# Optimization experiments

Hardware: AMD Instinct MI355X
Metric: run time of the kernel (lower is better)

Reference implementation:

```python
import jax, jax.numpy as jnp
import numpy as np

N_EMBD = 1024
N_HEAD = 16
HEAD_DIM = N_EMBD // N_HEAD


def setup_inputs() -> dict:
    key = jax.random.key(0)
    ks = jax.random.split(key, 9)
    B, S = 4, 2048
    s = 1.0 / np.sqrt(N_EMBD)
    return {
        "x": jax.random.normal(ks[0], (B, S, N_EMBD), dtype=jnp.float32),
        "attention_mask": jnp.ones((B, S), dtype=jnp.int32),
        "Wq": jax.random.normal(ks[1], (N_EMBD, N_EMBD), jnp.float32) * s,
        "bq": jnp.zeros((N_EMBD,), jnp.float32),
        "Wk": jax.random.normal(ks[2], (N_EMBD, N_EMBD), jnp.float32) * s,
        "bk": jnp.zeros((N_EMBD,), jnp.float32),
        "Wv": jax.random.normal(ks[3], (N_EMBD, N_EMBD), jnp.float32) * s,
        "bv": jnp.zeros((N_EMBD,), jnp.float32),
        "Wo": jax.random.normal(ks[4], (N_EMBD, N_EMBD), jnp.float32) * s,
        "bo": jnp.zeros((N_EMBD,), jnp.float32),
    }


def _split_heads(t):  # [B,S,E] -> [B,H,S,D]
    B, S, _ = t.shape
    return t.reshape(B, S, N_HEAD, HEAD_DIM).transpose(0, 2, 1, 3)


def reference(x, attention_mask, Wq, bq, Wk, bk, Wv, bv, Wo, bo):
    B, S, E = x.shape
    q = _split_heads(x @ Wq.T + bq)
    k = _split_heads(x @ Wk.T + bk)
    v = _split_heads(x @ Wv.T + bv)
    # scores: [B,H,S,S]
    scores = jnp.einsum('bhqd,bhkd->bhqk', q, k) / np.sqrt(HEAD_DIM).astype(np.float32)
    # additive mask: 0 where mask==1, -inf where mask==0, broadcast over heads/query
    mask = jnp.where(attention_mask[:, None, None, :] == 0, -jnp.inf, 0.0).astype(scores.dtype)
    scores = scores + mask
    probs = jax.nn.softmax(scores, axis=-1)  # dropout p=0 -> identity
    ctx = jnp.einsum('bhqk,bhkd->bhqd', probs, v)
    out = ctx.transpose(0, 2, 1, 3).reshape(B, S, E)
    return out @ Wo.T + bo
```

## Files before the change

kernel.cpp:

```cpp
#include <hip/hip_runtime.h>

typedef __bf16 bf16;
typedef __attribute__((ext_vector_type(2))) bf16 bf16x2;
typedef __attribute__((ext_vector_type(4))) bf16 bf16x4;
typedef __attribute__((ext_vector_type(8))) bf16 bf16x8;
typedef __attribute__((ext_vector_type(4))) float f32x4;
typedef __attribute__((ext_vector_type(16))) float f32x16;
typedef __attribute__((ext_vector_type(4))) int i32x4;
typedef __attribute__((ext_vector_type(2))) int i32x2;

#define MFMA_BF16(a, b, c) __builtin_amdgcn_mfma_f32_16x16x32_bf16((a), (b), (c), 0, 0, 0)
#define MFMA32(a, b, c)    __builtin_amdgcn_mfma_f32_32x32x16_bf16((a), (b), (c), 0, 0, 0)

constexpr int S_LEN = 2048;
constexpr int EMB   = 1024;
constexpr int NHEAD = 16;
constexpr int HDIM  = 64;
constexpr int BATCH = 4;
constexpr int NTOK  = BATCH * S_LEN;

__device__ __forceinline__ void gload_lds16(const bf16* g, bf16* l) {
    __builtin_amdgcn_global_load_lds(
        (const __attribute__((address_space(1))) void*)g,
        (__attribute__((address_space(3))) void*)l, 16, 0, 0);
}

__device__ __forceinline__ int pkbf(float a, float b) {
    bf16x2 t; t[0] = (bf16)a; t[1] = (bf16)b;
    return __builtin_bit_cast(int, t);
}

#if __has_builtin(__builtin_amdgcn_permlane32_swap)
__device__ __forceinline__ i32x2 permswap(int a, int b) {
    return __builtin_amdgcn_permlane32_swap(a, b, false, false);
}
#else
__device__ __forceinline__ i32x2 permswap(int a, int b) {
    int as = __shfl_xor(a, 32);
    int bs = __shfl_xor(b, 32);
    int hx_ = (threadIdx.x >> 5) & 1;
    i32x2 r;
    r[0] = hx_ ? bs : a;
    r[1] = hx_ ? b : as;
    return r;
}
#endif

__global__ __launch_bounds__(256)
void cvt_f32_bf16(const float* __restrict__ src, bf16* __restrict__ dst, int n4) {
    int i = blockIdx.x * 256 + threadIdx.x;
    if (i < n4) {
        f32x4 v = ((const f32x4*)src)[i];
        bf16x4 o;
        o[0] = (bf16)v[0]; o[1] = (bf16)v[1]; o[2] = (bf16)v[2]; o[3] = (bf16)v[3];
        ((bf16x4*)dst)[i] = o;
    }
}

__global__ __launch_bounds__(256)
void cvt_w4(const float* __restrict__ s0, const float* __restrict__ s1,
            const float* __restrict__ s2, const float* __restrict__ s3,
            bf16* __restrict__ dst) {
    const int a = blockIdx.y;
    const float* s = a == 0 ? s0 : (a == 1 ? s1 : (a == 2 ? s2 : s3));
    int i = blockIdx.x * 256 + threadIdx.x;
    f32x4 v = ((const f32x4*)s)[i];
    bf16x4 o;
    o[0] = (bf16)v[0]; o[1] = (bf16)v[1]; o[2] = (bf16)v[2]; o[3] = (bf16)v[3];
    ((bf16x4*)(dst + (size_t)a * EMB * EMB))[i] = o;
}

__global__ __launch_bounds__(512)
void gemm256(const bf16* __restrict__ A,
             const bf16* __restrict__ W0, const bf16* __restrict__ W1, const bf16* __restrict__ W2,
             const float* __restrict__ b0, const float* __restrict__ b1, const float* __restrict__ b2,
             void* __restrict__ d0, void* __restrict__ d1, void* __restrict__ d2,
             int fused, float q_scale)
{
    __shared__ bf16 lds[2][4][8192];

    int seg, mode, n0;
    if (fused) { seg = blockIdx.y >> 2; n0 = (blockIdx.y & 3) * 256; mode = (seg == 2) ? 1 : 0; }
    else       { seg = 0;              n0 = blockIdx.y * 256;        mode = 2; }
    const bf16*  W    = seg == 0 ? W0 : (seg == 1 ? W1 : W2);
    const float* bias = seg == 0 ? b0 : (seg == 1 ? b1 : b2);
    void*        C    = seg == 0 ? d0 : (seg == 1 ? d1 : d2);
    const float  osc  = (fused && seg == 0) ? q_scale : 1.0f;

    const int tid  = threadIdx.x;
    const int lane = tid & 63;
    const int w    = tid >> 6;
    const int wr   = w >> 2;
    const int wc   = w & 3;
    const int quad = lane >> 4;
    const int l16  = lane & 15;
    const int m0   = blockIdx.x * 256;

#define STAGE_A(BUF, H, T) {                                                        \
    _Pragma("unroll") for (int c_ = 0; c_ < 2; ++c_) {                              \
        int idx_ = c_ * 512 + tid;                                                  \
        int m_ = idx_ >> 2, s_ = idx_ & 3;                                          \
        gload_lds16(A + (size_t)(m0 + m_) * EMB + (T) * 64 + (H) * 32               \
                      + ((s_ ^ ((m_ >> 1) & 3)) << 3),                              \
                    &lds[BUF][H][idx_ * 8]);                                        \
    } }
#define STAGE_B(BUF, H, T) {                                                        \
    _Pragma("unroll") for (int c_ = 0; c_ < 2; ++c_) {                              \
        int idx_ = c_ * 512 + tid;                                                  \
        int n_ = idx_ >> 2, s_ = idx_ & 3;                                          \
        gload_lds16(W + (size_t)(n0 + n_) * EMB + (T) * 64 + (H) * 32               \
                      + ((s_ ^ ((n_ >> 1) & 3)) << 3),                              \
                    &lds[BUF][2 + (H)][idx_ * 8]);                                  \
    } }

#define READ_A(DST, BUF, H, G) {                                                    \
    _Pragma("unroll") for (int i_ = 0; i_ < 4; ++i_) {                              \
        int m_ = wr * 128 + (G) * 64 + i_ * 16 + l16;                               \
        DST[i_] = *(const bf16x8*)&lds[BUF][H][m_ * 32 + ((quad ^ ((m_ >> 1) & 3)) << 3)]; \
    } }
#define READ_B(DST, BUF, H) {                                                       \
    _Pragma("unroll") for (int j_ = 0; j_ < 4; ++j_) {                              \
        int n_ = wc * 64 + j_ * 16 + l16;                                           \
        DST[j_] = *(const bf16x8*)&lds[BUF][2 + (H)][n_ * 32 + ((quad ^ ((n_ >> 1) & 3)) << 3)]; \
    } }

#define MFMA_PH(AF, BF, G) {                                                        \
    __builtin_amdgcn_s_setprio(1);                                                  \
    _Pragma("unroll") for (int i_ = 0; i_ < 4; ++i_)                                \
        _Pragma("unroll") for (int j_ = 0; j_ < 4; ++j_)                            \
            acc[(G) * 4 + i_][j_] = MFMA_BF16(AF[i_], BF[j_], acc[(G) * 4 + i_][j_]); \
    __builtin_amdgcn_s_setprio(0);                                                  \
}

    f32x4 acc[8][4] = {};

    STAGE_A(0, 0, 0) STAGE_B(0, 0, 0) STAGE_A(0, 1, 0) STAGE_B(0, 1, 0)
    asm volatile("s_waitcnt vmcnt(4)" ::: "memory");
    __builtin_amdgcn_s_barrier();
    __builtin_amdgcn_sched_barrier(0);

    for (int t = 0; t < 16; ++t) {
        const int cur  = t & 1;
        const int nxt  = cur ^ 1;
        const bool more = (t + 1 < 16);
        bf16x8 afr[4], bfr[4];

        READ_B(bfr, cur, 0)
        READ_A(afr, cur, 0, 0)
        if (more) STAGE_A(nxt, 0, t + 1)
        MFMA_PH(afr, bfr, 0)

        READ_A(afr, cur, 0, 1)
        if (more) STAGE_B(nxt, 0, t + 1)
        MFMA_PH(afr, bfr, 1)
        if (more) asm volatile("s_waitcnt vmcnt(4)" ::: "memory");
        else      asm volatile("s_waitcnt vmcnt(0)" ::: "memory");
        __builtin_amdgcn_s_barrier();
        __builtin_amdgcn_sched_barrier(0);

        READ_B(bfr, cur, 1)
        READ_A(afr, cur, 1, 0)
        if (more) STAGE_A(nxt, 1, t + 1)
        MFMA_PH(afr, bfr, 0)

        READ_A(afr, cur, 1, 1)
        if (more) STAGE_B(nxt, 1, t + 1)
        MFMA_PH(afr, bfr, 1)
        if (more) {
            asm volatile("s_waitcnt vmcnt(4)" ::: "memory");
            __builtin_amdgcn_s_barrier();
            __builtin_amdgcn_sched_barrier(0);
        }
    }

#undef STAGE_A
#undef STAGE_B
#undef READ_A
#undef READ_B
#undef MFMA_PH

    #pragma unroll
    for (int ii = 0; ii < 8; ++ii) {
        #pragma unroll
        for (int j = 0; j < 4; ++j) {
            int col = n0 + wc * 64 + j * 16 + l16;
            float bv = bias[col];
            int row0 = m0 + wr * 128 + ii * 16 + quad * 4;
            if (mode == 1) {
                int bb = row0 >> 11, s0 = row0 & 2047;
                int hh = col >> 6,   d  = col & 63;
                bf16x4 pk;
                #pragma unroll
                for (int r = 0; r < 4; ++r) pk[r] = (bf16)(acc[ii][j][r] + bv);
                *(bf16x4*)((bf16*)C + (size_t)((bb * NHEAD + hh) * HDIM + d) * S_LEN + s0) = pk;
            } else if (mode == 0) {
                #pragma unroll
                for (int r = 0; r < 4; ++r)
                    ((bf16*)C)[(size_t)(row0 + r) * EMB + col] = (bf16)((acc[ii][j][r] + bv) * osc);
            } else {
                #pragma unroll
                for (int r = 0; r < 4; ++r)
                    ((float*)C)[(size_t)(row0 + r) * EMB + col] = acc[ii][j][r] + bv;
            }
        }
    }
}

__global__ __launch_bounds__(512)
void flash_attn(const bf16* __restrict__ qg, const bf16* __restrict__ kg,
                const bf16* __restrict__ vtg, const int* __restrict__ maskg,
                bf16* __restrict__ ctx)
{
    __shared__ bf16  klds[2][64 * 64];
    __shared__ bf16  vlds[2][64 * 64];
    __shared__ bf16  bias_lds[2048];
    __shared__ float stat_lds[8][32];

    const int fb  = blockIdx.x;
    const int xcd = fb & 7;
    const int rr  = fb >> 3;
    const int qi  = rr & 7;
    const int gg  = rr >> 3;
    const int g   = gg * 8 + xcd;
    const int h   = g & 15;
    const int b   = g >> 4;
    const int q0  = qi * 256;

    const int tid  = threadIdx.x;
    const int lane = tid & 63;
    const int w    = tid >> 6;
    const int l32  = lane & 31;
    const int hx   = lane >> 5;

    const int srow  = tid >> 3;
    const int sslot = (tid & 7) ^ (srow & 7);

    int ok;
    {
        int i = tid * 4;
        i32x4 mv = *(const i32x4*)(maskg + b * S_LEN + i);
        bf16x4 bb;
        ok = 1;
        #pragma unroll
        for (int r = 0; r < 4; ++r) {
            ok &= (mv[r] != 0);
            bb[r] = mv[r] ? (bf16)0.f : (bf16)(-3.0e38f);
        }
        *(bf16x4*)&bias_lds[i] = bb;
    }
    const int allvalid = __syncthreads_and(ok);

    bf16x8 qf[4];
    {
        const bf16* qrow = qg + (size_t)(b * S_LEN + q0 + w * 32 + l32) * EMB + h * HDIM + hx * 8;
        qf[0] = *(const bf16x8*)(qrow);
        qf[1] = *(const bf16x8*)(qrow + 16);
        qf[2] = *(const bf16x8*)(qrow + 32);
        qf[3] = *(const bf16x8*)(qrow + 48);
    }

    const bf16* kgb = kg  + (size_t)b * S_LEN * EMB + h * HDIM;
    const bf16* vgb = vtg + (size_t)((b * NHEAD + h) * HDIM) * S_LEN;

    float mrow = -1e30f, lpart = 0.f;
    f32x16 o0, o1;
    #pragma unroll
    for (int r = 0; r < 16; ++r) { o0[r] = 0.f; o1[r] = 0.f; }

#define STAGE(BUF, KT) {                                                            \
    gload_lds16(kgb + (size_t)((KT) * 64 + srow) * EMB + sslot * 8,                 \
                &klds[BUF][tid * 8]);                                               \
    gload_lds16(vgb + (size_t)srow * S_LEN + (KT) * 64 + sslot * 8,                 \
                &vlds[BUF][tid * 8]);                                               \
}

#define LDSK(CUR, ROW, SB) (*(const bf16x8*)((const char*)&klds[CUR][0] + ((ROW) << 7) + ((((SB) ^ ((ROW) & 7))) << 4)))
#define LDSV(CUR, ROW, SB) (*(const bf16x8*)((const char*)&vlds[CUR][0] + ((ROW) << 7) + ((((SB) ^ ((ROW) & 7))) << 4)))

#define SUBTILE(CUR, KT, KK) {                                                      \
    f32x16 s_;                                                                      \
    _Pragma("unroll") for (int r_ = 0; r_ < 16; ++r_) s_[r_] = 0.f;                 \
    const int krow_ = (KK) * 32 + l32;                                              \
    __builtin_amdgcn_s_setprio(1);                                                  \
    s_ = MFMA32(LDSK(CUR, krow_, 0 * 2 + hx), qf[0], s_);                           \
    s_ = MFMA32(LDSK(CUR, krow_, 1 * 2 + hx), qf[1], s_);                           \
    s_ = MFMA32(LDSK(CUR, krow_, 2 * 2 + hx), qf[2], s_);                           \
    s_ = MFMA32(LDSK(CUR, krow_, 3 * 2 + hx), qf[3], s_);                           \
    __builtin_amdgcn_s_setprio(0);                                                  \
    if (!allvalid) {                                                                \
        _Pragma("unroll") for (int s4_ = 0; s4_ < 4; ++s4_) {                       \
            bf16x4 b4_ = *(const bf16x4*)&bias_lds[(KT) * 64 + (KK) * 32 + s4_ * 8 + hx * 4]; \
            _Pragma("unroll") for (int t_ = 0; t_ < 4; ++t_)                        \
                s_[4 * s4_ + t_] += (float)b4_[t_];                                 \
        }                                                                           \
    }                                                                               \
    float rmax_ = s_[0];                                                            \
    _Pragma("unroll") for (int r_ = 1; r_ < 16; ++r_) rmax_ = fmaxf(rmax_, s_[r_]); \
    rmax_ = fmaxf(rmax_, __shfl_xor(rmax_, 32));                                    \
    if (!__all(rmax_ <= mrow + 8.f)) {                                              \
        float mnew_  = fmaxf(mrow, rmax_);                                          \
        float alpha_ = __builtin_amdgcn_exp2f(mrow - mnew_);                        \
        mrow = mnew_; lpart *= alpha_;                                              \
        if (hx == 0) stat_lds[w][l32] = alpha_;                                     \
        _Pragma("unroll") for (int s4_ = 0; s4_ < 4; ++s4_) {                       \
            f32x4 a4_ = *(const f32x4*)&stat_lds[w][s4_ * 8 + hx * 4];              \
            _Pragma("unroll") for (int t_ = 0; t_ < 4; ++t_) {                      \
                o0[4 * s4_ + t_] *= a4_[t_]; o1[4 * s4_ + t_] *= a4_[t_];           \
            }                                                                       \
        }                                                                           \
    }                                                                               \
    bf16x8 pa0, pa1;                                                                \
    {                                                                               \
        float p_[8];                                                                \
        _Pragma("unroll") for (int r_ = 0; r_ < 8; ++r_) {                          \
            p_[r_] = __builtin_amdgcn_exp2f(s_[r_] - mrow); lpart += p_[r_];        \
        }                                                                           \
        i32x2 r0_ = permswap(pkbf(p_[0], p_[1]), pkbf(p_[4], p_[5]));               \
        i32x2 r1_ = permswap(pkbf(p_[2], p_[3]), pkbf(p_[6], p_[7]));               \
        i32x4 fw_; fw_[0] = r0_[0]; fw_[1] = r1_[0]; fw_[2] = r0_[1]; fw_[3] = r1_[1]; \
        pa0 = __builtin_bit_cast(bf16x8, fw_);                                      \
    }                                                                               \
    {                                                                               \
        float p_[8];                                                                \
        _Pragma("unroll") for (int r_ = 0; r_ < 8; ++r_) {                          \
            p_[r_] = __builtin_amdgcn_exp2f(s_[8 + r_] - mrow); lpart += p_[r_];    \
        }                                                                           \
        i32x2 r0_ = permswap(pkbf(p_[0], p_[1]), pkbf(p_[4], p_[5]));               \
        i32x2 r1_ = permswap(pkbf(p_[2], p_[3]), pkbf(p_[6], p_[7]));               \
        i32x4 fw_; fw_[0] = r0_[0]; fw_[1] = r1_[0]; fw_[2] = r0_[1]; fw_[3] = r1_[1]; \
        pa1 = __builtin_bit_cast(bf16x8, fw_);                                      \
    }                                                                               \
    __builtin_amdgcn_s_setprio(1);                                                  \
    o0 = MFMA32(pa0, LDSV(CUR, 0 * 32 + l32, (KK) * 4 + 0 * 2 + hx), o0);           \
    o1 = MFMA32(pa0, LDSV(CUR, 1 * 32 + l32, (KK) * 4 + 0 * 2 + hx), o1);           \
    o0 = MFMA32(pa1, LDSV(CUR, 0 * 32 + l32, (KK) * 4 + 1 * 2 + hx), o0);           \
    o1 = MFMA32(pa1, LDSV(CUR, 1 * 32 + l32, (KK) * 4 + 1 * 2 + hx), o1);           \
    __builtin_amdgcn_s_setprio(0);                                                  \
}

    STAGE(0, 0)
    __syncthreads();

    for (int kt = 0; kt < 32; ++kt) {
        const int cur = kt & 1;
        if (kt + 1 < 32) STAGE(cur ^ 1, kt + 1)
        SUBTILE(cur, kt, 0)
        SUBTILE(cur, kt, 1)
        __syncthreads();
    }

#undef SUBTILE
#undef LDSK
#undef LDSV
#undef STAGE

    float lrow = lpart + __shfl_xor(lpart, 32);
    float inv  = lrow > 0.f ? 1.f / lrow : 0.f;
    if (hx == 0) stat_lds[w][l32] = inv;
    #pragma unroll
    for (int s4 = 0; s4 < 4; ++s4) {
        f32x4 i4 = *(const f32x4*)&stat_lds[w][s4 * 8 + hx * 4];
        #pragma unroll
        for (int t = 0; t < 4; ++t) {
            size_t row = (size_t)(b * S_LEN + q0 + w * 32 + s4 * 8 + hx * 4 + t);
            bf16* cp = ctx + row * EMB + h * HDIM + l32;
            cp[0]  = (bf16)(o0[4 * s4 + t] * i4[t]);
            cp[32] = (bf16)(o1[4 * s4 + t] * i4[t]);
        }
    }
}

extern "C" void kernel_launch(void* const* d_in, const int* in_sizes, int n_in,
                              void* d_out, int out_size, void* d_ws, size_t ws_size,
                              hipStream_t stream)
{
    const float* x   = (const float*)d_in[0];
    const int*  mask = (const int*)d_in[1];
    const float* Wq  = (const float*)d_in[2];
    const float* bq  = (const float*)d_in[3];
    const float* Wk  = (const float*)d_in[4];
    const float* bk  = (const float*)d_in[5];
    const float* Wv  = (const float*)d_in[6];
    const float* bv  = (const float*)d_in[7];
    const float* Wo  = (const float*)d_in[8];
    const float* bo  = (const float*)d_in[9];
    (void)in_sizes; (void)n_in; (void)out_size; (void)ws_size;

    const size_t me = (size_t)NTOK * EMB;
    const size_t we = (size_t)EMB * EMB;
    bf16* xb  = (bf16*)d_ws;
    bf16* qb  = xb  + me;
    bf16* kb  = qb  + me;
    bf16* vt  = kb  + me;
    bf16* wqb = vt  + me;
    bf16* wkb = wqb + we;
    bf16* wvb = wkb + we;
    bf16* wob = wvb + we;
    bf16* cx  = xb;

    cvt_f32_bf16<<<(int)(me / 4 / 256), 256, 0, stream>>>(x, xb, (int)(me / 4));
    cvt_w4<<<dim3((int)(we / 4 / 256), 4), 256, 0, stream>>>(Wq, Wk, Wv, Wo, wqb);

    gemm256<<<dim3(NTOK / 256, 12), 512, 0, stream>>>(
        xb, wqb, wkb, wvb, bq, bk, bv, qb, kb, vt, 1, 0.18033688011112042f);

    flash_attn<<<dim3(512), 512, 0, stream>>>(qb, kb, vt, mask, cx);

    gemm256<<<dim3(NTOK / 256, EMB / 256), 512, 0, stream>>>(
        cx, wob, wob, wob, bo, bo, bo, d_out, d_out, d_out, 0, 1.0f);
}
```

Measured before the change: 285.7 us.

## Shrink GEMM M-tile to 128 and remap blocks for XCD-aware L2 locality

Cuts the GEMM block tile from 256x256 to 128x256, halving the A staging and accumulator footprint per block and doubling the number of blocks. The QKV GEMM goes from 384 to 768 blocks and the output projection from 128 to 256, improving CU utilization on a 256-CU part. It also replaces the 2D grid with a 1D grid remapped so that consecutive blocks on the same XCD share M rows, aiming for better L2 reuse. In exchange, each block does less MFMA work per load, which lowers arithmetic intensity and re-reads the weight tiles more often.

```diff
diff --git a/kernel.cpp b/kernel.cpp
--- a/kernel.cpp
+++ b/kernel.cpp
@@ -77,11 +77,18 @@
              void* __restrict__ d0, void* __restrict__ d1, void* __restrict__ d2,
              int fused, float q_scale)
 {
-    __shared__ bf16 lds[2][4][8192];
+    __shared__ bf16 lds_a[2][2][128 * 32];
+    __shared__ bf16 lds_b[2][2][256 * 32];
+
+    const int fb  = blockIdx.x;
+    const int xcd = fb & 7;
+    const int loc = fb >> 3;
+    const int xi  = xcd * 8 + (loc & 7);
+    const int y   = loc >> 3;
 
     int seg, mode, n0;
-    if (fused) { seg = blockIdx.y >> 2; n0 = (blockIdx.y & 3) * 256; mode = (seg == 2) ? 1 : 0; }
-    else       { seg = 0;              n0 = blockIdx.y * 256;        mode = 2; }
+    if (fused) { seg = y >> 2; n0 = (y & 3) * 256; mode = (seg == 2) ? 1 : 0; }
+    else       { seg = 0;      n0 = y * 256;        mode = 2; }
     const bf16*  W    = seg == 0 ? W0 : (seg == 1 ? W1 : W2);
     const float* bias = seg == 0 ? b0 : (seg == 1 ? b1 : b2);
     void*        C    = seg == 0 ? d0 : (seg == 1 ? d1 : d2);
@@ -94,48 +101,46 @@
     const int wc   = w & 3;
     const int quad = lane >> 4;
     const int l16  = lane & 15;
-    const int m0   = blockIdx.x * 256;
+    const int m0   = xi * 128;
 
 #define STAGE_A(BUF, H, T) {                                                        \
-    _Pragma("unroll") for (int c_ = 0; c_ < 2; ++c_) {                              \
-        int idx_ = c_ * 512 + tid;                                                  \
-        int m_ = idx_ >> 2, s_ = idx_ & 3;                                          \
-        gload_lds16(A + (size_t)(m0 + m_) * EMB + (T) * 64 + (H) * 32               \
-                      + ((s_ ^ ((m_ >> 1) & 3)) << 3),                              \
-                    &lds[BUF][H][idx_ * 8]);                                        \
-    } }
+    int m_ = tid >> 2, s_ = tid & 3;                                                \
+    gload_lds16(A + (size_t)(m0 + m_) * EMB + (T) * 64 + (H) * 32                   \
+                  + ((s_ ^ ((m_ >> 1) & 3)) << 3),                                  \
+                &lds_a[BUF][H][tid * 8]);                                           \
+}
 #define STAGE_B(BUF, H, T) {                                                        \
     _Pragma("unroll") for (int c_ = 0; c_ < 2; ++c_) {                              \
         int idx_ = c_ * 512 + tid;                                                  \
         int n_ = idx_ >> 2, s_ = idx_ & 3;                                          \
         gload_lds16(W + (size_t)(n0 + n_) * EMB + (T) * 64 + (H) * 32               \
                       + ((s_ ^ ((n_ >> 1) & 3)) << 3),                              \
-                    &lds[BUF][2 + (H)][idx_ * 8]);                                  \
+                    &lds_b[BUF][H][idx_ * 8]);                                      \
     } }
 
 #define READ_A(DST, BUF, H, G) {                                                    \
-    _Pragma("unroll") for (int i_ = 0; i_ < 4; ++i_) {                              \
-        int m_ = wr * 128 + (G) * 64 + i_ * 16 + l16;                               \
-        DST[i_] = *(const bf16x8*)&lds[BUF][H][m_ * 32 + ((quad ^ ((m_ >> 1) & 3)) << 3)]; \
+    _Pragma("unroll") for (int i_ = 0; i_ < 2; ++i_) {                              \
+        int m_ = wr * 64 + (G) * 32 + i_ * 16 + l16;                                \
+        DST[i_] = *(const bf16x8*)&lds_a[BUF][H][m_ * 32 + ((quad ^ ((m_ >> 1) & 3)) << 3)]; \
     } }
 #define READ_B(DST, BUF, H) {                                                       \
     _Pragma("unroll") for (int j_ = 0; j_ < 4; ++j_) {                              \
         int n_ = wc * 64 + j_ * 16 + l16;                                           \
-        DST[j_] = *(const bf16x8*)&lds[BUF][2 + (H)][n_ * 32 + ((quad ^ ((n_ >> 1) & 3)) << 3)]; \
+        DST[j_] = *(const bf16x8*)&lds_b[BUF][H][n_ * 32 + ((quad ^ ((n_ >> 1) & 3)) << 3)]; \
     } }
 
 #define MFMA_PH(AF, BF, G) {                                                        \
     __builtin_amdgcn_s_setprio(1);                                                  \
-    _Pragma("unroll") for (int i_ = 0; i_ < 4; ++i_)                                \
+    _Pragma("unroll") for (int i_ = 0; i_ < 2; ++i_)                                \
         _Pragma("unroll") for (int j_ = 0; j_ < 4; ++j_)                            \
-            acc[(G) * 4 + i_][j_] = MFMA_BF16(AF[i_], BF[j_], acc[(G) * 4 + i_][j_]); \
+            acc[(G) * 2 + i_][j_] = MFMA_BF16(AF[i_], BF[j_], acc[(G) * 2 + i_][j_]); \
     __builtin_amdgcn_s_setprio(0);                                                  \
 }
 
-    f32x4 acc[8][4] = {};
+    f32x4 acc[4][4] = {};
 
     STAGE_A(0, 0, 0) STAGE_B(0, 0, 0) STAGE_A(0, 1, 0) STAGE_B(0, 1, 0)
-    asm volatile("s_waitcnt vmcnt(4)" ::: "memory");
+    asm volatile("s_waitcnt vmcnt(3)" ::: "memory");
     __builtin_amdgcn_s_barrier();
     __builtin_amdgcn_sched_barrier(0);
 
@@ -143,7 +148,7 @@
         const int cur  = t & 1;
         const int nxt  = cur ^ 1;
         const bool more = (t + 1 < 16);
-        bf16x8 afr[4], bfr[4];
+        bf16x8 afr[2], bfr[4];
 
         READ_B(bfr, cur, 0)
         READ_A(afr, cur, 0, 0)
@@ -153,7 +158,7 @@
         READ_A(afr, cur, 0, 1)
         if (more) STAGE_B(nxt, 0, t + 1)
         MFMA_PH(afr, bfr, 1)
-        if (more) asm volatile("s_waitcnt vmcnt(4)" ::: "memory");
+        if (more) asm volatile("s_waitcnt vmcnt(3)" ::: "memory");
         else      asm volatile("s_waitcnt vmcnt(0)" ::: "memory");
         __builtin_amdgcn_s_barrier();
         __builtin_amdgcn_sched_barrier(0);
@@ -167,7 +172,7 @@
         if (more) STAGE_B(nxt, 1, t + 1)
         MFMA_PH(afr, bfr, 1)
         if (more) {
-            asm volatile("s_waitcnt vmcnt(4)" ::: "memory");
+            asm volatile("s_waitcnt vmcnt(3)" ::: "memory");
             __builtin_amdgcn_s_barrier();
             __builtin_amdgcn_sched_barrier(0);
         }
@@ -180,12 +185,12 @@
 #undef MFMA_PH
 
     #pragma unroll
-    for (int ii = 0; ii < 8; ++ii) {
+    for (int ii = 0; ii < 4; ++ii) {
         #pragma unroll
         for (int j = 0; j < 4; ++j) {
             int col = n0 + wc * 64 + j * 16 + l16;
             float bv = bias[col];
-            int row0 = m0 + wr * 128 + ii * 16 + quad * 4;
+            int row0 = m0 + wr * 64 + ii * 16 + quad * 4;
             if (mode == 1) {
                 int bb = row0 >> 11, s0 = row0 & 2047;
                 int hh = col >> 6,   d  = col & 63;
@@ -401,11 +406,11 @@
     cvt_f32_bf16<<<(int)(me / 4 / 256), 256, 0, stream>>>(x, xb, (int)(me / 4));
     cvt_w4<<<dim3((int)(we / 4 / 256), 4), 256, 0, stream>>>(Wq, Wk, Wv, Wo, wqb);
 
-    gemm256<<<dim3(NTOK / 256, 12), 512, 0, stream>>>(
+    gemm256<<<dim3(64 * 12), 512, 0, stream>>>(
         xb, wqb, wkb, wvb, bq, bk, bv, qb, kb, vt, 1, 0.18033688011112042f);
 
     flash_attn<<<dim3(512), 512, 0, stream>>>(qb, kb, vt, mask, cx);
 
-    gemm256<<<dim3(NTOK / 256, EMB / 256), 512, 0, stream>>>(
+    gemm256<<<dim3(64 * 4), 512, 0, stream>>>(
         cx, wob, wob, wob, bo, bo, bo, d_out, d_out, d_out, 0, 1.0f);
 }
```

Measured after the change: 297.7 us. 4.2% more time.
